# Performance work log

Measured on AMD Instinct MI355X. Metric: run time of the kernel, lower is better.

The kernel has to match this reference:

```python
import jax, jax.numpy as jnp
import numpy as np

BN_EPS = 1e-5
N_EULER = 8


def _bn_train(x, gamma, beta):
    # BatchNorm1d in training mode: biased batch statistics over the batch axis
    mu = jnp.mean(x, axis=0)
    var = jnp.mean((x - mu) ** 2, axis=0)
    return gamma * (x - mu) / jnp.sqrt(var + BN_EPS) + beta


def setup_inputs() -> dict:
    key = jax.random.key(0)
    ks = jax.random.split(key, 16)
    B, d, u_dim, n_obs, sdim = 4096, 512, 64, 25, 128
    h1, h2, hd = 1024, 1024, 512

    def w(k, shape, fan_in):
        return jax.random.normal(k, shape, dtype=jnp.float32) / np.sqrt(fan_in)

    return {
        "z_dyn": jax.random.normal(ks[0], (B, d), dtype=jnp.float32),
        "z_static": jax.random.normal(ks[1], (B, sdim), dtype=jnp.float32),
        "dt": jnp.array(0.05, dtype=jnp.float32),
        "ut": jax.random.normal(ks[2], (B, u_dim), dtype=jnp.float32),
        "eps": jax.random.normal(ks[3], (N_EULER, B, d), dtype=jnp.float32),
        "W1": w(ks[4], (h1, d), d), "b1": jnp.zeros((h1,), jnp.float32),
        "g1": jnp.ones((h1,), jnp.float32), "be1": jnp.zeros((h1,), jnp.float32),
        "W2": w(ks[5], (h2, h1), h1), "b2": jnp.zeros((h2,), jnp.float32),
        "g2": jnp.ones((h2,), jnp.float32), "be2": jnp.zeros((h2,), jnp.float32),
        "W3": w(ks[6], (d, h2), h2), "b3": jnp.zeros((d,), jnp.float32),
        "Wd1": w(ks[7], (hd, d), d), "bd1": jnp.zeros((hd,), jnp.float32),
        "Wd2": w(ks[8], (d, hd), hd), "bd2": jnp.zeros((d,), jnp.float32),
        "B_sde": w(ks[9], (d, u_dim), u_dim),
        "C": w(ks[10], (n_obs, d), d),
        "D": w(ks[11], (n_obs, u_dim), u_dim),
    }


def reference(z_dyn, z_static, dt, ut, eps,
              W1, b1, g1, be1, W2, b2, g2, be2, W3, b3,
              Wd1, bd1, Wd2, bd2, B_sde, C, D):
    h = dt / N_EULER
    sqrt_h = jnp.sqrt(jnp.abs(h) + 1e-8)

    def drift(z):
        a = jax.nn.relu(_bn_train(z @ W1.T + b1, g1, be1))
        a = jax.nn.relu(_bn_train(a @ W2.T + b2, g2, be2))
        return a @ W3.T + b3

    def diffusion(z):
        t = jnp.tanh(z @ Wd1.T + bd1)
        return jax.nn.softplus(t @ Wd2.T + bd2) + 1e-5

    def step(z, e):
        f = drift(z)
        g = diffusion(z)
        z = z + h * f + sqrt_h * g * e  # Euler-Maruyama update (training mode)
        return z, None

    z, _ = jax.lax.scan(step, z_dyn, eps)
    ut_dt = ut * dt
    z_next = z + ut_dt @ B_sde.T
    yt = z_next @ C.T + ut_dt @ D.T
    return (z_next, yt)
```

## Files before the change

### kernel.cpp

```cpp
#include <hip/hip_runtime.h>


typedef unsigned short ushort_t;
typedef __bf16 bf16x8 __attribute__((ext_vector_type(8)));
typedef _Float16 f16x8 __attribute__((ext_vector_type(8)));
typedef float f32x4 __attribute__((ext_vector_type(4)));

__device__ __forceinline__ float bf2f(ushort_t s) {
  unsigned u = ((unsigned)s) << 16;
  return __uint_as_float(u);
}
__device__ __forceinline__ ushort_t f2bf(float f) {
  unsigned u = __float_as_uint(f);
  unsigned lsb = (u >> 16) & 1u;
  u += 0x7fffu + lsb;
  return (ushort_t)(u >> 16);
}
__device__ __forceinline__ float ldin(const void* p, size_t i, int f32) {
  return f32 ? ((const float*)p)[i] : bf2f(((const ushort_t*)p)[i]);
}
__device__ __forceinline__ void async16(const void* g, void* l) {
  __builtin_amdgcn_global_load_lds(
      (const __attribute__((address_space(1))) void*)g,
      (__attribute__((address_space(3))) void*)l, 16, 0, 0);
}

template <int N>
__device__ __forceinline__ void waitvm() {
  if constexpr (N == 0) {
    asm volatile("s_waitcnt vmcnt(0)" ::: "memory");
  } else if constexpr (N == 4) {
    asm volatile("s_waitcnt vmcnt(4)" ::: "memory");
  } else if constexpr (N == 6) {
    asm volatile("s_waitcnt vmcnt(6)" ::: "memory");
  }
  __builtin_amdgcn_sched_barrier(0);
}
__device__ __forceinline__ void waitlgkm0() {
  asm volatile("s_waitcnt lgkmcnt(0)" ::: "memory");
  __builtin_amdgcn_sched_barrier(0);
}

__device__ __forceinline__ bf16x8 lds_frag(const __bf16* T, int row, int kb) {
  const int byte = (row << 7) + ((((kb >> 3) ^ (row & 7))) << 4);
  return *(const bf16x8*)((const char*)T + byte);
}

__global__ void k_detect(const void* __restrict__ eps, const void* __restrict__ dtraw,
                         float* __restrict__ consts) {
  __shared__ float mx[256];
  const int t = threadIdx.x;
  const ushort_t* e = (const ushort_t*)eps;
  float m = 0.f;
#pragma unroll
  for (int k = 0; k < 4; ++k) {
    float v = fabsf(bf2f(e[t * 4 + k]));
    if (!(v < 1e30f)) v = 1e30f;
    m = fmaxf(m, v);
  }
  mx[t] = m;
  __syncthreads();
  if (t == 0) {
    float M = 0.f;
    for (int k = 0; k < 256; ++k) M = fmaxf(M, mx[k]);
    const int f32 = (M > 1e3f) ? 1 : 0;
    float dt;
    if (f32) {
      dt = *(const float*)dtraw;
    } else {
      float db = bf2f(*(const ushort_t*)dtraw);
      float df = *(const float*)dtraw;
      dt = (db > 1e-6f && db < 1e3f) ? db : df;
    }
    const float h = dt * 0.125f;
    consts[0] = h;
    consts[1] = sqrtf(fabsf(h) + 1e-8f);
    consts[2] = dt;
    consts[3] = (float)f32;
  }
}

struct ConvArgs { const void* src[5]; };
#define CONV_TOT 2621440

__global__ __launch_bounds__(256) void k_prep(
    ConvArgs a, const float* __restrict__ consts, ushort_t* __restrict__ canon,
    const void* __restrict__ z, float* __restrict__ zf,
    ushort_t* __restrict__ zb, const void* __restrict__ ut,
    const void* __restrict__ Bsde, float* __restrict__ Ub,
    const void* __restrict__ Cm, const void* __restrict__ Dm,
    float* __restrict__ Deff, float* __restrict__ stats) {
  __shared__ float smem[2 * 64 * 68];
  const int f32 = consts[3] != 0.f;
  const int b = blockIdx.x;
  const int t = threadIdx.x;

  if (b < 2560) {
    constexpr int CUM[6] = {0, 524288, 786432, 1835008, 2359296, 2621440};
    const int i = (b * 256 + t) * 4;
    if (i >= CONV_TOT) return;
    int j = 0;
#pragma unroll
    for (int k = 1; k < 5; ++k)
      if (i >= CUM[k]) j = k;
    const int local = i - CUM[j];
    const void* s = a.src[j];
    ushort4 o;
    if (f32) {
      float4 v = ((const float4*)s)[local >> 2];
      o = make_ushort4(f2bf(v.x), f2bf(v.y), f2bf(v.z), f2bf(v.w));
    } else {
      o = ((const ushort4*)s)[local >> 2];
    }
    *(ushort4*)(canon + i) = o;
  } else if (b < 4608) {
    const int i = (b - 2560) * 256 + t;
    float4 v;
    if (f32) {
      v = ((const float4*)z)[i];
    } else {
      ushort4 u = ((const ushort4*)z)[i];
      v = make_float4(bf2f(u.x), bf2f(u.y), bf2f(u.z), bf2f(u.w));
    }
    ((float4*)zf)[i] = v;
    ((ushort4*)zb)[i] =
        make_ushort4(f2bf(v.x), f2bf(v.y), f2bf(v.z), f2bf(v.w));
  } else if (b < 5120) {
    float(*As)[68] = (float(*)[68])smem;
    float(*Bs)[68] = (float(*)[68])(smem + 64 * 68);
    const float dt = consts[2];
    const int bb = b - 4608;
    const int n0 = (bb & 7) * 64, m0 = (bb >> 3) * 64;
    const int tx = t & 15, ty = t >> 4;
    const int r = t >> 2;
    const int c0 = (t & 3) * 16;
#pragma unroll
    for (int j = 0; j < 16; ++j) {
      As[c0 + j][r] = ldin(ut, (size_t)(m0 + r) * 64 + c0 + j, f32);
      Bs[c0 + j][r] = ldin(Bsde, (size_t)(n0 + r) * 64 + c0 + j, f32);
    }
    __syncthreads();
    float acc[4][4] = {};
#pragma unroll 8
    for (int kk = 0; kk < 64; ++kk) {
      float av[4], bv[4];
      *(float4*)av = *(const float4*)&As[kk][ty * 4];
      *(float4*)bv = *(const float4*)&Bs[kk][tx * 4];
#pragma unroll
      for (int i = 0; i < 4; ++i)
#pragma unroll
        for (int j = 0; j < 4; ++j) acc[i][j] += av[i] * bv[j];
    }
#pragma unroll
    for (int i = 0; i < 4; ++i) {
      const size_t o = (size_t)(m0 + ty * 4 + i) * 512 + n0 + tx * 4;
      *(float4*)&Ub[o] = make_float4(dt * acc[i][0], dt * acc[i][1],
                                     dt * acc[i][2], dt * acc[i][3]);
    }
  } else if (b < 5145) {
    float(*red)[64] = (float(*)[64])smem;
    const int j = b - 5120;
    const int k = t & 63;
    const int part = t >> 6;
    float acc = 0.f;
    const int l0 = part * 128;
#pragma unroll 8
    for (int l = l0; l < l0 + 128; ++l)
      acc += ldin(Cm, (size_t)j * 512 + l, f32) *
             ldin(Bsde, (size_t)l * 64 + k, f32);
    red[part][k] = acc;
    __syncthreads();
    if (part == 0) {
      float s = red[0][k] + red[1][k] + red[2][k] + red[3][k];
      Deff[j * 64 + k] = s + ldin(Dm, (size_t)j * 64 + k, f32);
    }
  } else {
    const int i = ((b - 5145) * 256 + t) * 4;
    *(float4*)&stats[i] = make_float4(0.f, 0.f, 0.f, 0.f);
  }
}

template <int MT, int KT, int MODE, int STATS, int FUSE, int BIAS, int FINAL,
          int ANORM, int DEEP>
__device__ __forceinline__ void gemm_body(
    const ushort_t* __restrict__ A, const ushort_t* __restrict__ W,
    const void* __restrict__ bias, int ncol0, ushort_t* __restrict__ Cout,
    int Nout, int m0, int n0, __bf16* As, __bf16* Bs,
    float* __restrict__ s1, float* __restrict__ s2,
    const ushort_t* __restrict__ Gb, float* __restrict__ zf,
    ushort_t* __restrict__ zb, const void* __restrict__ eps,
    unsigned long long eoff, const float* __restrict__ consts,
    const float* __restrict__ Ub, float* __restrict__ out0,
    const float* __restrict__ s1in, const float* __restrict__ s2in,
    const void* __restrict__ gsc, const void* __restrict__ gbe,
    _Float16* scF, _Float16* shF, float* sS) {
  constexpr int BM = MT * 64;
  constexpr int LPT = MT * 2 + 2;
  const int f32 = consts[3] != 0.f;
  const int tid = threadIdx.x;
  const int lane = tid & 63;
  const int wave = tid >> 6;
  const int col = lane & 15;
  const int quad = lane >> 4;
  const int rowBase = wave * (MT * 16);

  const int srow = tid >> 3;
  const int skc = tid & 7;
  auto stageA = [&](int k0, __bf16* dst) {
#pragma unroll
    for (int j = 0; j < BM / 32; ++j) {
      const int row = j * 32 + srow;
      async16(A + (size_t)(m0 + row) * KT + k0 + (((skc ^ (row & 7))) << 3),
              (char*)dst + (j * 256 + tid) * 16);
    }
  };
  auto stageB = [&](int k0, __bf16* dst) {
#pragma unroll
    for (int j = 0; j < 2; ++j) {
      const int row = j * 32 + srow;
      async16(W + (size_t)(n0 + row) * KT + k0 + (((skc ^ (row & 7))) << 3),
              (char*)dst + (j * 256 + tid) * 16);
    }
  };

  auto tables = [&]() {
    if (ANORM) {
      const float inv = 1.0f / 4096.0f;
#pragma unroll
      for (int c0 = 0; c0 < KT; c0 += 256) {
        const int c = c0 + tid;
        float mu = s1in[c] * inv;
        float var = fmaxf(s2in[c] * inv - mu * mu, 0.f);
        float sc = ldin(gsc, c, f32) * rsqrtf(var + 1e-5f);
        scF[c] = (_Float16)sc;
        shF[c] = (_Float16)(ldin(gbe, c, f32) - mu * sc);
      }
    }
  };

  f32x4 acc[MT][4] = {};
  constexpr int NIT = KT / 64;

  auto computeTile = [&](const __bf16* Ac, const __bf16* Bc, int k0) {
#pragma unroll
    for (int kk = 0; kk < 2; ++kk) {
      const int kb = kk * 32 + quad * 8;
      bf16x8 af[MT], bfr[4];
      if (ANORM) {
        f16x8 scv = *(const f16x8*)&scF[k0 + kb];
        f16x8 shv = *(const f16x8*)&shF[k0 + kb];
#pragma unroll
        for (int mt = 0; mt < MT; ++mt) {
          bf16x8 raw = lds_frag(Ac, rowBase + mt * 16 + col, kb);
#pragma unroll
          for (int j = 0; j < 8; ++j)
            af[mt][j] = (__bf16)fmaxf(
                fmaf((float)raw[j], (float)scv[j], (float)shv[j]), 0.f);
        }
      } else {
#pragma unroll
        for (int mt = 0; mt < MT; ++mt)
          af[mt] = lds_frag(Ac, rowBase + mt * 16 + col, kb);
      }
#pragma unroll
      for (int nt = 0; nt < 4; ++nt)
        bfr[nt] = lds_frag(Bc, nt * 16 + col, kb);
      __builtin_amdgcn_s_setprio(1);
#pragma unroll
      for (int mt = 0; mt < MT; ++mt)
#pragma unroll
        for (int nt = 0; nt < 4; ++nt)
          acc[mt][nt] = __builtin_amdgcn_mfma_f32_16x16x32_bf16(
              af[mt], bfr[nt], acc[mt][nt], 0, 0, 0);
      __builtin_amdgcn_s_setprio(0);
    }
  };

  if (DEEP) {
    __bf16* Ac = As;
    __bf16* An = As + BM * 64;
    __bf16* A2 = As + 2 * BM * 64;
    __bf16* Bc = Bs;
    __bf16* Bn = Bs + 64 * 64;
    __bf16* B2 = Bs + 2 * 64 * 64;
    stageA(0, Ac);
    stageB(0, Bc);
    stageA(64, An);
    stageB(64, Bn);
    tables();
    waitlgkm0();
#pragma unroll 1
    for (int it = 0; it < NIT; ++it) {
      if (it + 1 < NIT) {
        waitvm<LPT>();
      } else {
        waitvm<0>();
      }
      __builtin_amdgcn_s_barrier();
      if (it + 2 < NIT) {
        stageA((it + 2) * 64, A2);
        stageB((it + 2) * 64, B2);
      }
      computeTile(Ac, Bc, it * 64);
      __bf16* ta = Ac; Ac = An; An = A2; A2 = ta;
      __bf16* tb = Bc; Bc = Bn; Bn = B2; B2 = tb;
    }
  } else {
    __bf16* Acur = As;
    __bf16* Aalt = As + BM * 64;
    __bf16* Bcur = Bs;
    __bf16* Balt = Bs + 64 * 64;
    stageA(0, Acur);
    stageB(0, Bcur);
    tables();
    waitlgkm0();
    __builtin_amdgcn_s_barrier();
#pragma unroll 1
    for (int it = 0; it < NIT; ++it) {
      const int k0 = it * 64;
      if (it + 1 < NIT) {
        stageA(k0 + 64, Aalt);
        stageB(k0 + 64, Balt);
        waitvm<LPT>();
      } else {
        waitvm<0>();
      }
      __builtin_amdgcn_s_barrier();
      computeTile(Acur, Bcur, k0);
      waitlgkm0();
      __builtin_amdgcn_s_barrier();
      __bf16* t0 = Acur; Acur = Aalt; Aalt = t0;
      __bf16* t1 = Bcur; Bcur = Balt; Balt = t1;
    }
  }

  if (STATS) {
    for (int i = tid; i < 128; i += 256) sS[i] = 0.f;
    __syncthreads();
  }

  const float h = consts[0], sh = consts[1];

#pragma unroll
  for (int nt = 0; nt < 4; ++nt) {
    const int gn = n0 + nt * 16 + col;
    const float bv = BIAS ? ldin(bias, gn + ncol0, f32) : 0.f;
    float ls = 0.f, lq = 0.f;
#pragma unroll
    for (int mt = 0; mt < MT; ++mt) {
#pragma unroll
      for (int r = 0; r < 4; ++r) {
        const int gm = m0 + rowBase + mt * 16 + quad * 4 + r;
        float v = acc[mt][nt][r] + bv;
        if (STATS) {
          ls += v;
          lq += v * v;
        }
        if (MODE == 1) {
          v = tanhf(v);
        } else if (MODE == 2) {
          v = fmaxf(v, 0.f) + log1pf(expf(-fabsf(v))) + 1e-5f;
        }
        const size_t o = (size_t)gm * Nout + gn + ncol0;
        if (FUSE) {
          const float e = ldin(eps, eoff + o, f32);
          const float g = bf2f(Gb[o]);
          const float z = zf[o] + h * v + sh * g * e;
          zf[o] = z;
          zb[o] = f2bf(z);
          if (FINAL) out0[o] = z + Ub[o];
        } else {
          Cout[o] = f2bf(v);
        }
      }
    }
    if (STATS) {
      atomicAdd(&sS[nt * 16 + col], ls);
      atomicAdd(&sS[64 + nt * 16 + col], lq);
    }
  }

  if (STATS) {
    __syncthreads();
    if (tid < 64) {
      atomicAdd(&s1[n0 + tid], sS[tid]);
      atomicAdd(&s2[n0 + tid], sS[64 + tid]);
    }
  }
}

__global__ __launch_bounds__(256, 3) void k_x1t(
    const ushort_t* __restrict__ zb, const ushort_t* __restrict__ Wcat,
    const void* __restrict__ bd1, ushort_t* __restrict__ Xb,
    ushort_t* __restrict__ Tb, float* __restrict__ s1, float* __restrict__ s2,
    const float* __restrict__ consts) {
  __shared__ __bf16 As[2 * 128 * 64] __attribute__((aligned(16)));
  __shared__ __bf16 Bs[2 * 64 * 64] __attribute__((aligned(16)));
  __shared__ float sS[128];
  const int L = blockIdx.x;
  const int q = L & 7, w = L >> 3;
  const int mloc = w & 3, n = w >> 2;
  const int m0 = (q * 4 + mloc) * 128;
  const int n0 = n * 64;
  if (n < 16) {
    gemm_body<2, 512, 0, 1, 0, 0, 0, 0, 0>(
        zb, Wcat, nullptr, 0, Xb, 1024, m0, n0, As, Bs, s1, s2, nullptr,
        nullptr, nullptr, nullptr, 0, consts, nullptr, nullptr, nullptr,
        nullptr, nullptr, nullptr, nullptr, nullptr, sS);
  } else {
    gemm_body<2, 512, 1, 0, 0, 1, 0, 0, 0>(
        zb, Wcat, bd1, -1024, Tb, 512, m0, n0, As, Bs, nullptr,
        nullptr, nullptr, nullptr, nullptr, nullptr, 0, consts, nullptr,
        nullptr, nullptr, nullptr, nullptr, nullptr, nullptr, nullptr, sS);
  }
}

__global__ __launch_bounds__(256, 3) void k_x2g(
    const ushort_t* __restrict__ X1raw, const ushort_t* __restrict__ W2c,
    const ushort_t* __restrict__ Tb, const ushort_t* __restrict__ Wd2c,
    const void* __restrict__ bd2, ushort_t* __restrict__ Ab,
    ushort_t* __restrict__ Gb, float* __restrict__ s1o, float* __restrict__ s2o,
    const float* __restrict__ s1i, const float* __restrict__ s2i,
    const void* __restrict__ g1, const void* __restrict__ be1,
    const float* __restrict__ consts) {
  __shared__ __bf16 As[2 * 128 * 64] __attribute__((aligned(16)));
  __shared__ __bf16 Bs[2 * 64 * 64] __attribute__((aligned(16)));
  __shared__ _Float16 scF[1024] __attribute__((aligned(16)));
  __shared__ _Float16 shF[1024] __attribute__((aligned(16)));
  __shared__ float sS[128];
  const int L = blockIdx.x;
  if (L < 512) {
    const int q = L & 7, w = L >> 3;
    const int mloc = w & 3, n = w >> 2;
    const int m0 = (q * 4 + mloc) * 128, n0 = n * 64;
    gemm_body<2, 1024, 0, 1, 0, 0, 0, 1, 0>(
        X1raw, W2c, nullptr, 0, Ab, 1024, m0, n0, As, Bs, s1o, s2o,
        nullptr, nullptr, nullptr, nullptr, 0, consts, nullptr, nullptr, s1i,
        s2i, g1, be1, scF, shF, sS);
  } else {
    const int Lg = L - 512;
    const int q = Lg & 7, w = Lg >> 3;
    const int mloc = w & 3, n = w >> 2;
    const int m0 = (q * 4 + mloc) * 128, n0 = n * 64;
    gemm_body<2, 512, 2, 0, 0, 1, 0, 0, 0>(
        Tb, Wd2c, bd2, 0, Gb, 512, m0, n0, As, Bs, nullptr, nullptr,
        nullptr, nullptr, nullptr, nullptr, 0, consts, nullptr, nullptr,
        nullptr, nullptr, nullptr, nullptr, nullptr, nullptr, sS);
  }
}

template <int FINAL>
__global__ __launch_bounds__(256, 2) void k_fupd(
    const ushort_t* __restrict__ X2raw, const ushort_t* __restrict__ W3c,
    const void* __restrict__ b3, const ushort_t* __restrict__ Gb,
    float* __restrict__ zf, ushort_t* __restrict__ zb,
    const void* __restrict__ eps, unsigned long long eoff,
    const float* __restrict__ consts, const float* __restrict__ Ub,
    float* __restrict__ out0, const float* __restrict__ s1i,
    const float* __restrict__ s2i, const void* __restrict__ g2,
    const void* __restrict__ be2) {
  __shared__ __bf16 As[3 * 64 * 64] __attribute__((aligned(16)));
  __shared__ __bf16 Bs[3 * 64 * 64] __attribute__((aligned(16)));
  __shared__ _Float16 scF[1024] __attribute__((aligned(16)));
  __shared__ _Float16 shF[1024] __attribute__((aligned(16)));
  const int L = blockIdx.x;
  const int q = L & 7, w = L >> 3;
  const int mloc = w & 7, n = w >> 3;
  const int m0 = (q * 8 + mloc) * 64, n0 = n * 64;
  gemm_body<1, 1024, 0, 0, 1, 1, FINAL, 1, 1>(
      X2raw, W3c, b3, 0, nullptr, 512, m0, n0, As, Bs, nullptr, nullptr,
      Gb, zf, zb, eps, eoff, consts, Ub, out0, s1i, s2i, g2, be2, scF, shF,
      nullptr);
}

__global__ __launch_bounds__(256) void k_final2(
    const float* __restrict__ zf, const void* __restrict__ ut,
    const float* __restrict__ consts, const void* __restrict__ Cm,
    const float* __restrict__ Deff, float* __restrict__ out1) {
  const float dt = consts[2];
  const int f32 = consts[3] != 0.f;
  const int t = threadIdx.x;
  const int lane = t & 63;
  const int m = blockIdx.x * 4 + (t >> 6);
  float z8[8];
#pragma unroll
  for (int i = 0; i < 8; ++i) z8[i] = zf[(size_t)m * 512 + i * 64 + lane];
  const float u = ldin(ut, (size_t)m * 64 + lane, f32);

  for (int j = 0; j < 25; ++j) {
    float p = dt * u * Deff[j * 64 + lane];
#pragma unroll
    for (int i = 0; i < 8; ++i)
      p += z8[i] * ldin(Cm, (size_t)j * 512 + i * 64 + lane, f32);
#pragma unroll
    for (int off = 32; off > 0; off >>= 1) p += __shfl_down(p, off, 64);
    if (lane == 0) out1[m * 25 + j] = p;
  }
}

extern "C" void kernel_launch(void* const* d_in, const int* in_sizes, int n_in,
                              void* d_out, int out_size, void* d_ws, size_t ws_size,
                              hipStream_t stream) {
  static const int expA[22] = {
      2097152, 524288, 1,      262144, 16777216, 524288, 1024, 1024,
      1024,    1048576, 1024,  1024,   1024,     524288, 512,  262144,
      512,     262144, 512,    32768,  12800,    1600};

  int map[21];
  bool okA = (n_in == 22), okB = (n_in == 21);
  if (okA)
    for (int i = 0; i < 22; ++i)
      if (in_sizes[i] != expA[i]) { okA = false; break; }
  if (okB) {
    int j = 0;
    for (int i = 0; i < 22; ++i) {
      if (i == 1) continue;
      if (in_sizes[j] != expA[i]) { okB = false; break; }
      ++j;
    }
  }
  if (okA) {
    map[0] = 0;
    for (int i = 1; i < 21; ++i) map[i] = i + 1;
  } else if (okB) {
    for (int i = 0; i < 21; ++i) map[i] = i;
  } else {
    map[0] = 0;
    for (int i = 1; i < 21; ++i) map[i] = (i + 1 < n_in) ? i + 1 : n_in - 1;
  }

  const void* z_dyn = d_in[map[0]];
  const void* dtp = d_in[map[1]];
  const void* ut = d_in[map[2]];
  const void* eps = d_in[map[3]];
  const void* W1 = d_in[map[4]];
  const void* g1 = d_in[map[6]];
  const void* be1 = d_in[map[7]];
  const void* W2 = d_in[map[8]];
  const void* g2 = d_in[map[10]];
  const void* be2 = d_in[map[11]];
  const void* W3 = d_in[map[12]];
  const void* b3 = d_in[map[13]];
  const void* Wd1 = d_in[map[14]];
  const void* bd1 = d_in[map[15]];
  const void* Wd2 = d_in[map[16]];
  const void* bd2 = d_in[map[17]];
  const void* Bsde = d_in[map[18]];
  const void* Cm = d_in[map[19]];
  const void* Dm = d_in[map[20]];

  char* ws = (char*)d_ws;
  const size_t MB = 1024 * 1024;
  float* zf = (float*)(ws + 0);
  ushort_t* zb = (ushort_t*)(ws + 8 * MB);
  ushort_t* Xb = (ushort_t*)(ws + 12 * MB);
  ushort_t* Ab = (ushort_t*)(ws + 20 * MB);
  ushort_t* Tb = (ushort_t*)(ws + 28 * MB);
  ushort_t* Gb = (ushort_t*)(ws + 32 * MB);
  float* Ub = (float*)(ws + 36 * MB);
  ushort_t* canon = (ushort_t*)(ws + 44 * MB);
  float* stats = (float*)(ws + 49 * MB + 512 * 1024);
  float* consts = stats + 16 * 2048;
  float* Deff = consts + 16;

  const ushort_t* Wcat = canon + 0;
  const ushort_t* W2c = canon + 786432;
  const ushort_t* W3c = canon + 1835008;
  const ushort_t* Wd2c = canon + 2359296;

  float* out_z = (float*)d_out;
  float* out_y = out_z + 4096 * 512;

  const dim3 blk(256);

  k_detect<<<1, blk, 0, stream>>>(eps, dtp, consts);

  ConvArgs ca;
  ca.src[0] = W1;
  ca.src[1] = Wd1;
  ca.src[2] = W2;
  ca.src[3] = W3;
  ca.src[4] = Wd2;

  k_prep<<<5177, blk, 0, stream>>>(ca, consts, canon, z_dyn, zf, zb, ut,
                                   Bsde, Ub, Cm, Dm, Deff, stats);

  for (int s = 0; s < 8; ++s) {
    float* sA1 = stats + (s * 2 + 0) * 2048;
    float* sA2 = stats + (s * 2 + 1) * 2048;
    const unsigned long long eoff = (unsigned long long)s * 4096 * 512;

    k_x1t<<<768, blk, 0, stream>>>(zb, Wcat, bd1, Xb, Tb,
                                   sA1, sA1 + 1024, consts);

    k_x2g<<<768, blk, 0, stream>>>(Xb, W2c, Tb, Wd2c, bd2, Ab, Gb,
                                   sA2, sA2 + 1024, sA1, sA1 + 1024,
                                   g1, be1, consts);

    if (s < 7) {
      k_fupd<0><<<512, blk, 0, stream>>>(Ab, W3c, b3, Gb, zf, zb, eps, eoff,
                                         consts, Ub, out_z, sA2, sA2 + 1024,
                                         g2, be2);
    } else {
      k_fupd<1><<<512, blk, 0, stream>>>(Ab, W3c, b3, Gb, zf, zb, eps, eoff,
                                         consts, Ub, out_z, sA2, sA2 + 1024,
                                         g2, be2);
    }
  }

  k_final2<<<1024, blk, 0, stream>>>(zf, ut, consts, Cm, Deff, out_y);
}
```

Measured before the change: 750.6 us.

## Split GEMM tiles across eight waves per block in x1t and x2g

Generalizes the GEMM body so the wave count per block is a template parameter. The 128-row tiles in k_x1t and k_x2g are now computed by 8 waves of one 16-row strip each (512 threads) instead of 4 waves of two strips. Per-wave accumulator and fragment registers shrink and more waves are available to hide latency. The cost is that each wave reuses its B fragments across fewer MFMAs, so there are more LDS reads per MFMA and more barrier participants.

```diff
diff --git a/kernel.cpp b/kernel.cpp
--- a/kernel.cpp
+++ b/kernel.cpp
@@ -29,6 +29,8 @@
 __device__ __forceinline__ void waitvm() {
   if constexpr (N == 0) {
     asm volatile("s_waitcnt vmcnt(0)" ::: "memory");
+  } else if constexpr (N == 3) {
+    asm volatile("s_waitcnt vmcnt(3)" ::: "memory");
   } else if constexpr (N == 4) {
     asm volatile("s_waitcnt vmcnt(4)" ::: "memory");
   } else if constexpr (N == 6) {
@@ -180,8 +182,8 @@
   }
 }
 
-template <int MT, int KT, int MODE, int STATS, int FUSE, int BIAS, int FINAL,
-          int ANORM, int DEEP>
+template <int MTW, int WV, int KT, int MODE, int STATS, int FUSE, int BIAS,
+          int FINAL, int ANORM, int DEEP>
 __device__ __forceinline__ void gemm_body(
     const ushort_t* __restrict__ A, const ushort_t* __restrict__ W,
     const void* __restrict__ bias, int ncol0, ushort_t* __restrict__ Cout,
@@ -194,32 +196,35 @@
     const float* __restrict__ s1in, const float* __restrict__ s2in,
     const void* __restrict__ gsc, const void* __restrict__ gbe,
     _Float16* scF, _Float16* shF, float* sS) {
-  constexpr int BM = MT * 64;
-  constexpr int LPT = MT * 2 + 2;
+  constexpr int BM = MTW * WV * 16;
+  constexpr int NTH = WV * 64;
+  constexpr int ASH = BM / (8 * WV);
+  constexpr int BSH = 64 / (8 * WV);
+  constexpr int LPT = ASH + BSH;
   const int f32 = consts[3] != 0.f;
   const int tid = threadIdx.x;
   const int lane = tid & 63;
   const int wave = tid >> 6;
   const int col = lane & 15;
   const int quad = lane >> 4;
-  const int rowBase = wave * (MT * 16);
+  const int rowBase = wave * (MTW * 16);
 
   const int srow = tid >> 3;
   const int skc = tid & 7;
   auto stageA = [&](int k0, __bf16* dst) {
 #pragma unroll
-    for (int j = 0; j < BM / 32; ++j) {
-      const int row = j * 32 + srow;
+    for (int j = 0; j < ASH; ++j) {
+      const int row = j * (WV * 8) + srow;
       async16(A + (size_t)(m0 + row) * KT + k0 + (((skc ^ (row & 7))) << 3),
-              (char*)dst + (j * 256 + tid) * 16);
+              (char*)dst + (j * NTH + tid) * 16);
     }
   };
   auto stageB = [&](int k0, __bf16* dst) {
 #pragma unroll
-    for (int j = 0; j < 2; ++j) {
-      const int row = j * 32 + srow;
+    for (int j = 0; j < BSH; ++j) {
+      const int row = j * (WV * 8) + srow;
       async16(W + (size_t)(n0 + row) * KT + k0 + (((skc ^ (row & 7))) << 3),
-              (char*)dst + (j * 256 + tid) * 16);
+              (char*)dst + (j * NTH + tid) * 16);
     }
   };
 
@@ -227,30 +232,32 @@
     if (ANORM) {
       const float inv = 1.0f / 4096.0f;
 #pragma unroll
-      for (int c0 = 0; c0 < KT; c0 += 256) {
+      for (int c0 = 0; c0 < KT; c0 += NTH) {
         const int c = c0 + tid;
-        float mu = s1in[c] * inv;
-        float var = fmaxf(s2in[c] * inv - mu * mu, 0.f);
-        float sc = ldin(gsc, c, f32) * rsqrtf(var + 1e-5f);
-        scF[c] = (_Float16)sc;
-        shF[c] = (_Float16)(ldin(gbe, c, f32) - mu * sc);
+        if (c < KT) {
+          float mu = s1in[c] * inv;
+          float var = fmaxf(s2in[c] * inv - mu * mu, 0.f);
+          float sc = ldin(gsc, c, f32) * rsqrtf(var + 1e-5f);
+          scF[c] = (_Float16)sc;
+          shF[c] = (_Float16)(ldin(gbe, c, f32) - mu * sc);
+        }
       }
     }
   };
 
-  f32x4 acc[MT][4] = {};
+  f32x4 acc[MTW][4] = {};
   constexpr int NIT = KT / 64;
 
   auto computeTile = [&](const __bf16* Ac, const __bf16* Bc, int k0) {
 #pragma unroll
     for (int kk = 0; kk < 2; ++kk) {
       const int kb = kk * 32 + quad * 8;
-      bf16x8 af[MT], bfr[4];
+      bf16x8 af[MTW], bfr[4];
       if (ANORM) {
         f16x8 scv = *(const f16x8*)&scF[k0 + kb];
         f16x8 shv = *(const f16x8*)&shF[k0 + kb];
 #pragma unroll
-        for (int mt = 0; mt < MT; ++mt) {
+        for (int mt = 0; mt < MTW; ++mt) {
           bf16x8 raw = lds_frag(Ac, rowBase + mt * 16 + col, kb);
 #pragma unroll
           for (int j = 0; j < 8; ++j)
@@ -259,7 +266,7 @@
         }
       } else {
 #pragma unroll
-        for (int mt = 0; mt < MT; ++mt)
+        for (int mt = 0; mt < MTW; ++mt)
           af[mt] = lds_frag(Ac, rowBase + mt * 16 + col, kb);
       }
 #pragma unroll
@@ -267,7 +274,7 @@
         bfr[nt] = lds_frag(Bc, nt * 16 + col, kb);
       __builtin_amdgcn_s_setprio(1);
 #pragma unroll
-      for (int mt = 0; mt < MT; ++mt)
+      for (int mt = 0; mt < MTW; ++mt)
 #pragma unroll
         for (int nt = 0; nt < 4; ++nt)
           acc[mt][nt] = __builtin_amdgcn_mfma_f32_16x16x32_bf16(
@@ -335,7 +342,7 @@
   }
 
   if (STATS) {
-    for (int i = tid; i < 128; i += 256) sS[i] = 0.f;
+    for (int i = tid; i < 128; i += NTH) sS[i] = 0.f;
     __syncthreads();
   }
 
@@ -347,7 +354,7 @@
     const float bv = BIAS ? ldin(bias, gn + ncol0, f32) : 0.f;
     float ls = 0.f, lq = 0.f;
 #pragma unroll
-    for (int mt = 0; mt < MT; ++mt) {
+    for (int mt = 0; mt < MTW; ++mt) {
 #pragma unroll
       for (int r = 0; r < 4; ++r) {
         const int gm = m0 + rowBase + mt * 16 + quad * 4 + r;
@@ -389,7 +396,7 @@
   }
 }
 
-__global__ __launch_bounds__(256, 3) void k_x1t(
+__global__ __launch_bounds__(512, 6) void k_x1t(
     const ushort_t* __restrict__ zb, const ushort_t* __restrict__ Wcat,
     const void* __restrict__ bd1, ushort_t* __restrict__ Xb,
     ushort_t* __restrict__ Tb, float* __restrict__ s1, float* __restrict__ s2,
@@ -403,19 +410,19 @@
   const int m0 = (q * 4 + mloc) * 128;
   const int n0 = n * 64;
   if (n < 16) {
-    gemm_body<2, 512, 0, 1, 0, 0, 0, 0, 0>(
+    gemm_body<1, 8, 512, 0, 1, 0, 0, 0, 0, 0>(
         zb, Wcat, nullptr, 0, Xb, 1024, m0, n0, As, Bs, s1, s2, nullptr,
         nullptr, nullptr, nullptr, 0, consts, nullptr, nullptr, nullptr,
         nullptr, nullptr, nullptr, nullptr, nullptr, sS);
   } else {
-    gemm_body<2, 512, 1, 0, 0, 1, 0, 0, 0>(
+    gemm_body<1, 8, 512, 1, 0, 0, 1, 0, 0, 0>(
         zb, Wcat, bd1, -1024, Tb, 512, m0, n0, As, Bs, nullptr,
         nullptr, nullptr, nullptr, nullptr, nullptr, 0, consts, nullptr,
         nullptr, nullptr, nullptr, nullptr, nullptr, nullptr, nullptr, sS);
   }
 }
 
-__global__ __launch_bounds__(256, 3) void k_x2g(
+__global__ __launch_bounds__(512, 6) void k_x2g(
     const ushort_t* __restrict__ X1raw, const ushort_t* __restrict__ W2c,
     const ushort_t* __restrict__ Tb, const ushort_t* __restrict__ Wd2c,
     const void* __restrict__ bd2, ushort_t* __restrict__ Ab,
@@ -433,7 +440,7 @@
     const int q = L & 7, w = L >> 3;
     const int mloc = w & 3, n = w >> 2;
     const int m0 = (q * 4 + mloc) * 128, n0 = n * 64;
-    gemm_body<2, 1024, 0, 1, 0, 0, 0, 1, 0>(
+    gemm_body<1, 8, 1024, 0, 1, 0, 0, 0, 1, 0>(
         X1raw, W2c, nullptr, 0, Ab, 1024, m0, n0, As, Bs, s1o, s2o,
         nullptr, nullptr, nullptr, nullptr, 0, consts, nullptr, nullptr, s1i,
         s2i, g1, be1, scF, shF, sS);
@@ -442,7 +449,7 @@
     const int q = Lg & 7, w = Lg >> 3;
     const int mloc = w & 3, n = w >> 2;
     const int m0 = (q * 4 + mloc) * 128, n0 = n * 64;
-    gemm_body<2, 512, 2, 0, 0, 1, 0, 0, 0>(
+    gemm_body<1, 8, 512, 2, 0, 0, 1, 0, 0, 0>(
         Tb, Wd2c, bd2, 0, Gb, 512, m0, n0, As, Bs, nullptr, nullptr,
         nullptr, nullptr, nullptr, nullptr, 0, consts, nullptr, nullptr,
         nullptr, nullptr, nullptr, nullptr, nullptr, nullptr, sS);
@@ -467,7 +474,7 @@
   const int q = L & 7, w = L >> 3;
   const int mloc = w & 7, n = w >> 3;
   const int m0 = (q * 8 + mloc) * 64, n0 = n * 64;
-  gemm_body<1, 1024, 0, 0, 1, 1, FINAL, 1, 1>(
+  gemm_body<1, 4, 1024, 0, 0, 1, 1, FINAL, 1, 1>(
       X2raw, W3c, b3, 0, nullptr, 512, m0, n0, As, Bs, nullptr, nullptr,
       Gb, zf, zb, eps, eoff, consts, Ub, out0, s1i, s2i, g2, be2, scF, shF,
       nullptr);
@@ -572,6 +579,7 @@
   float* out_y = out_z + 4096 * 512;
 
   const dim3 blk(256);
+  const dim3 blk512(512);
 
   k_detect<<<1, blk, 0, stream>>>(eps, dtp, consts);
 
@@ -590,12 +598,12 @@
     float* sA2 = stats + (s * 2 + 1) * 2048;
     const unsigned long long eoff = (unsigned long long)s * 4096 * 512;
 
-    k_x1t<<<768, blk, 0, stream>>>(zb, Wcat, bd1, Xb, Tb,
-                                   sA1, sA1 + 1024, consts);
-
-    k_x2g<<<768, blk, 0, stream>>>(Xb, W2c, Tb, Wd2c, bd2, Ab, Gb,
-                                   sA2, sA2 + 1024, sA1, sA1 + 1024,
-                                   g1, be1, consts);
+    k_x1t<<<768, blk512, 0, stream>>>(zb, Wcat, bd1, Xb, Tb,
+                                      sA1, sA1 + 1024, consts);
+
+    k_x2g<<<768, blk512, 0, stream>>>(Xb, W2c, Tb, Wd2c, bd2, Ab, Gb,
+                                      sA2, sA2 + 1024, sA1, sA1 + 1024,
+                                      g1, be1, consts);
 
     if (s < 7) {
       k_fupd<0><<<512, blk, 0, stream>>>(Ab, W3c, b3, Gb, zf, zb, eps, eoff,
```

After: 822.7 us. +9.6%, slower.
